# Performance work log

Measured on AMD Instinct MI355X. Metric: run time of the kernel, lower is better.

Reference implementation:

```python
import jax, jax.numpy as jnp
import numpy as np

N, E, F_IN, H, O = 50000, 800000, 128, 64, 1


def _gcn_conv(x, row, col, ew, W, b, n_nodes):
    """PyG GCNConv: add self-loops (weight 1), symmetric deg normalization,
    linear transform (no bias inside lin), scatter-add aggregation, then +bias."""
    loop = jnp.arange(n_nodes, dtype=row.dtype)
    r = jnp.concatenate([row, loop])
    c = jnp.concatenate([col, loop])
    w = jnp.concatenate([ew, jnp.ones((n_nodes,), dtype=ew.dtype)])
    deg = jax.ops.segment_sum(w, c, num_segments=n_nodes)            # [N]
    dis = jnp.where(deg > 0, jax.lax.rsqrt(jnp.maximum(deg, 1e-12)), 0.0)
    norm = dis[r] * w * dis[c]                                       # [E+N]
    h = x @ W                                                        # [N, out]
    msg = h[r] * norm[:, None]                                       # gather + scale
    agg = jax.ops.segment_sum(msg, c, num_segments=n_nodes)          # scatter-add
    return agg + b


def setup_inputs() -> dict:
    key = jax.random.key(0)
    ks = jax.random.split(key, 14)
    s = 0.02
    return {
        "x": jax.random.normal(ks[0], (N, F_IN), dtype=jnp.float32),
        "edge_index": jax.random.randint(ks[1], (2, E), 0, N, dtype=jnp.int64),
        "edge_weight": jax.random.uniform(ks[2], (E,), dtype=jnp.float32),
        "W1": jax.random.normal(ks[3], (F_IN, H), dtype=jnp.float32) * s,
        "b1": jnp.zeros((H,), dtype=jnp.float32),
        "W2": jax.random.normal(ks[4], (H, H), dtype=jnp.float32) * s,
        "b2": jnp.zeros((H,), dtype=jnp.float32),
        "W_ih": jax.random.normal(ks[5], (4 * H, H), dtype=jnp.float32) * s,
        "W_hh": jax.random.normal(ks[6], (4 * H, H), dtype=jnp.float32) * s,
        "b_ih": jax.random.normal(ks[7], (4 * H,), dtype=jnp.float32) * s,
        "b_hh": jax.random.normal(ks[8], (4 * H,), dtype=jnp.float32) * s,
        "W_reg": jax.random.normal(ks[9], (H, O), dtype=jnp.float32) * s,
        "b_reg": jnp.zeros((O,), dtype=jnp.float32),
    }


def reference(x, edge_index, edge_weight, W1, b1, W2, b2,
              W_ih, W_hh, b_ih, b_hh, W_reg, b_reg):
    row, col = edge_index[0], edge_index[1]
    n = x.shape[0]
    h = jax.nn.relu(_gcn_conv(x, row, col, edge_weight, W1, b1, n))
    h = jax.nn.relu(_gcn_conv(h, row, col, edge_weight, W2, b2, n))
    # single-step LSTM, zero initial (h0, c0); PyTorch gate order i, f, g, o
    hd = W_ih.shape[1]
    h0 = jnp.zeros((n, hd), dtype=h.dtype)
    gates = h @ W_ih.T + h0 @ W_hh.T + b_ih + b_hh                   # [N, 4H]
    i, f, g, o = jnp.split(gates, 4, axis=-1)
    c = jax.nn.sigmoid(f) * 0.0 + jax.nn.sigmoid(i) * jnp.tanh(g)    # c0 = 0
    hn = jax.nn.sigmoid(o) * jnp.tanh(c)                             # lstm_out[:, -1]
    return hn @ W_reg + b_reg
```

## Files before the change

kernel.cpp:

```cpp
#include <hip/hip_runtime.h>
#include <math.h>


#define QN 6272
#define NOCT 8
#define NPAD (NOCT * QN)
#define NSLICE 128
#define HIST_BLOCKS (NSLICE * NOCT)

__device__ __forceinline__ float sigmoidf_(float x) {
    return 1.0f / (1.0f + expf(-x));
}

__global__ __launch_bounds__(256) void hist_gemm1_k(
        const int* __restrict__ col, unsigned short* __restrict__ part,
        int E, int N,
        const float* __restrict__ x, const float* __restrict__ W1,
        float* __restrict__ C) {
    extern __shared__ char smem[];
    const int t = threadIdx.x;
    if (blockIdx.x < HIST_BLOCKS) {
        int* hc = (int*)smem;
        const int s = blockIdx.x >> 3;
        const int q = blockIdx.x & 7;
        const int lo = q * QN;
        for (int i = t; i < QN; i += 256) hc[i] = 0;
        __syncthreads();
        const int per = (E + NSLICE - 1) / NSLICE;
        const int e0 = s * per, e1 = min(E, e0 + per);
        int e = e0 + t;
        for (; e + 768 < e1; e += 1024) {
            int c0 = col[e], c1 = col[e + 256], c2 = col[e + 512], c3 = col[e + 768];
            unsigned r0 = (unsigned)(c0 - lo), r1 = (unsigned)(c1 - lo);
            unsigned r2 = (unsigned)(c2 - lo), r3 = (unsigned)(c3 - lo);
            if (r0 < (unsigned)QN && (unsigned)c0 < (unsigned)N) atomicAdd(&hc[r0], 1);
            if (r1 < (unsigned)QN && (unsigned)c1 < (unsigned)N) atomicAdd(&hc[r1], 1);
            if (r2 < (unsigned)QN && (unsigned)c2 < (unsigned)N) atomicAdd(&hc[r2], 1);
            if (r3 < (unsigned)QN && (unsigned)c3 < (unsigned)N) atomicAdd(&hc[r3], 1);
        }
        for (; e < e1; e += 256) {
            int c = col[e];
            unsigned rel = (unsigned)(c - lo);
            if (rel < (unsigned)QN && (unsigned)c < (unsigned)N) atomicAdd(&hc[rel], 1);
        }
        __syncthreads();
        unsigned short* dst = part + (size_t)s * NPAD + lo;
        for (int i = t; i < QN; i += 256) dst[i] = (unsigned short)hc[i];
    } else {
        float (*xs)[68] = (float (*)[68])smem;
        float* ws = (float*)(smem + 64 * 68 * sizeof(float));
        const int n0 = (int)(blockIdx.x - HIST_BLOCKS) * 64;
        for (int base = t * 4; base < 128 * 64; base += 1024)
            *(float4*)(ws + base) = *(const float4*)(W1 + base);
        const int cg = t & 15, ng = t >> 4;
        const int colj = cg * 4, nb = ng * 4;
        float acc[4][4];
#pragma unroll
        for (int i = 0; i < 4; ++i)
#pragma unroll
            for (int j = 0; j < 4; ++j) acc[i][j] = 0.0f;
        for (int k0 = 0; k0 < 128; k0 += 64) {
            __syncthreads();
            for (int base = t * 4; base < 64 * 64; base += 1024) {
                int r = base >> 6, k = base & 63;
                int node = n0 + r;
                float4 v = make_float4(0.f, 0.f, 0.f, 0.f);
                if (node < N) v = *(const float4*)(x + (size_t)node * 128 + k0 + k);
                *(float4*)&xs[r][k] = v;
            }
            __syncthreads();
#pragma unroll 4
            for (int kk = 0; kk < 64; kk += 4) {
                float4 a[4];
#pragma unroll
                for (int i = 0; i < 4; ++i) a[i] = *(float4*)&xs[nb + i][kk];
#pragma unroll
                for (int j = 0; j < 4; ++j) {
                    float4 bv = *(float4*)&ws[(size_t)(k0 + kk + j) * 64 + colj];
                    float av[4];
                    switch (j) {
                        case 0: av[0]=a[0].x; av[1]=a[1].x; av[2]=a[2].x; av[3]=a[3].x; break;
                        case 1: av[0]=a[0].y; av[1]=a[1].y; av[2]=a[2].y; av[3]=a[3].y; break;
                        case 2: av[0]=a[0].z; av[1]=a[1].z; av[2]=a[2].z; av[3]=a[3].z; break;
                        default:av[0]=a[0].w; av[1]=a[1].w; av[2]=a[2].w; av[3]=a[3].w; break;
                    }
#pragma unroll
                    for (int i = 0; i < 4; ++i) {
                        acc[i][0] = fmaf(av[i], bv.x, acc[i][0]);
                        acc[i][1] = fmaf(av[i], bv.y, acc[i][1]);
                        acc[i][2] = fmaf(av[i], bv.z, acc[i][2]);
                        acc[i][3] = fmaf(av[i], bv.w, acc[i][3]);
                    }
                }
            }
        }
#pragma unroll
        for (int i = 0; i < 4; ++i) {
            int node = n0 + nb + i;
            if (node < N)
                *(float4*)(C + (size_t)node * 64 + colj) =
                    make_float4(acc[i][0], acc[i][1], acc[i][2], acc[i][3]);
        }
    }
}

__global__ __launch_bounds__(256) void prefixA_k(const unsigned short* __restrict__ part,
                                                 unsigned short* __restrict__ coff,
                                                 int* __restrict__ cnt,
                                                 int* __restrict__ bsum) {
    __shared__ int r[256];
    const int t = threadIdx.x;
    const int i = blockIdx.x * 256 + t;
    int acc = 0;
    for (int s = 0; s < NSLICE; ++s) {
        size_t idx = (size_t)s * NPAD + i;
        coff[idx] = (unsigned short)acc;
        acc += part[idx];
    }
    cnt[i] = acc;
    r[t] = acc;
    __syncthreads();
#pragma unroll
    for (int off = 128; off > 0; off >>= 1) {
        if (t < off) r[t] += r[t + off];
        __syncthreads();
    }
    if (t == 0) bsum[blockIdx.x] = r[0];
}

__global__ __launch_bounds__(256) void scanBC_k(const int* __restrict__ cnt,
                                                const int* __restrict__ bsum,
                                                int* __restrict__ rowptr, int NBLK) {
    __shared__ int s[2][256];
    __shared__ int red[256];
    const int t = threadIdx.x, b = blockIdx.x;
    const int i = b * 256 + t;
    int v = cnt[i];
    int pin = 0;
    s[0][t] = v;
    __syncthreads();
#pragma unroll
    for (int off = 1; off < 256; off <<= 1) {
        int xo = s[pin][t];
        if (t >= off) xo += s[pin][t - off];
        s[pin ^ 1][t] = xo;
        pin ^= 1;
        __syncthreads();
    }
    int excl = s[pin][t] - v;
    red[t] = (t < b && t < NBLK) ? bsum[t] : 0;
    __syncthreads();
#pragma unroll
    for (int off = 128; off > 0; off >>= 1) {
        if (t < off) red[t] += red[t + off];
        __syncthreads();
    }
    rowptr[i] = excl + red[0];
}

__global__ __launch_bounds__(256) void fill_k(const int* __restrict__ row,
                                              const int* __restrict__ col,
                                              const float* __restrict__ ew,
                                              const int* __restrict__ rowptr,
                                              const unsigned short* __restrict__ coff,
                                              int2* __restrict__ pairs, int E, int N) {
    __shared__ int lcur[QN];
    const int t = threadIdx.x;
    const int s = blockIdx.x >> 3;
    const int q = blockIdx.x & 7;
    const int lo = q * QN;
    const unsigned short* cof = coff + (size_t)s * NPAD + lo;
    const int* rp = rowptr + lo;
    for (int i = t; i < QN; i += 256) lcur[i] = rp[i] + (int)cof[i];
    __syncthreads();
    const int per = (E + NSLICE - 1) / NSLICE;
    const int e0 = s * per, e1 = min(E, e0 + per);
    int e = e0 + t;
    for (; e + 768 < e1; e += 1024) {
        int c0 = col[e], c1 = col[e + 256], c2 = col[e + 512], c3 = col[e + 768];
        unsigned r0 = (unsigned)(c0 - lo), r1 = (unsigned)(c1 - lo);
        unsigned r2 = (unsigned)(c2 - lo), r3 = (unsigned)(c3 - lo);
        if (r0 < (unsigned)QN && (unsigned)c0 < (unsigned)N) {
            int r = row[e]; float w = ew[e];
            if ((unsigned)r >= (unsigned)N) { r = 0; w = 0.0f; }
            pairs[atomicAdd(&lcur[r0], 1)] = make_int2(r, __float_as_int(w));
        }
        if (r1 < (unsigned)QN && (unsigned)c1 < (unsigned)N) {
            int r = row[e + 256]; float w = ew[e + 256];
            if ((unsigned)r >= (unsigned)N) { r = 0; w = 0.0f; }
            pairs[atomicAdd(&lcur[r1], 1)] = make_int2(r, __float_as_int(w));
        }
        if (r2 < (unsigned)QN && (unsigned)c2 < (unsigned)N) {
            int r = row[e + 512]; float w = ew[e + 512];
            if ((unsigned)r >= (unsigned)N) { r = 0; w = 0.0f; }
            pairs[atomicAdd(&lcur[r2], 1)] = make_int2(r, __float_as_int(w));
        }
        if (r3 < (unsigned)QN && (unsigned)c3 < (unsigned)N) {
            int r = row[e + 768]; float w = ew[e + 768];
            if ((unsigned)r >= (unsigned)N) { r = 0; w = 0.0f; }
            pairs[atomicAdd(&lcur[r3], 1)] = make_int2(r, __float_as_int(w));
        }
    }
    for (; e < e1; e += 256) {
        int c = col[e];
        unsigned rel = (unsigned)(c - lo);
        if (rel < (unsigned)QN && (unsigned)c < (unsigned)N) {
            int r = row[e]; float w = ew[e];
            if ((unsigned)r >= (unsigned)N) { r = 0; w = 0.0f; }
            pairs[atomicAdd(&lcur[rel], 1)] = make_int2(r, __float_as_int(w));
        }
    }
}

__global__ __launch_bounds__(256) void degsum_k(const int* __restrict__ rowptr,
                                                const int2* __restrict__ pairs,
                                                float* __restrict__ dis, int N) {
    int i = blockIdx.x * 256 + threadIdx.x;
    if (i >= N) return;
    int b = rowptr[i], en = rowptr[i + 1];
    float s = 0.0f;
    for (int e = b; e < en; ++e) s += __int_as_float(pairs[e].y);
    dis[i] = rsqrtf(s + 1.0f);
}

__global__ __launch_bounds__(256) void aggregate_k(const float* __restrict__ h,
                                                   const int* __restrict__ rowptr,
                                                   const int2* __restrict__ pairs,
                                                   const float* __restrict__ dis,
                                                   const float* __restrict__ bias,
                                                   float* __restrict__ out, int N) {
    __shared__ int2 pl[4][4][64];
    const int t = threadIdx.x;
    const int lane = t & 63, w = t >> 6;
    const int n0 = (blockIdx.x * 4 + w) * 4;
    if (n0 >= N) return;

    int rp[5];
#pragma unroll
    for (int k = 0; k < 5; ++k) rp[k] = rowptr[min(n0 + k, N)];
    int len[4]; int L = 0;
#pragma unroll
    for (int i = 0; i < 4; ++i) { len[i] = rp[i + 1] - rp[i]; L = max(L, len[i]); }

    float acc[4] = {0.f, 0.f, 0.f, 0.f};
    for (int base = 0; base < L; base += 64) {
#pragma unroll
        for (int i = 0; i < 4; ++i) {
            int m = len[i] - base;
            int2 p = make_int2(0, 0);
            if (lane < m) {
                p = pairs[rp[i] + base + lane];
                p.y = __float_as_int(__int_as_float(p.y) * dis[p.x]);
            }
            pl[w][i][lane] = p;
        }
        const int m = min(64, L - base);
        int j = 0;
        for (; j + 4 <= m; j += 4) {
#pragma unroll
            for (int jj = 0; jj < 4; ++jj) {
                int2 p0 = pl[w][0][j + jj];
                int2 p1 = pl[w][1][j + jj];
                int2 p2 = pl[w][2][j + jj];
                int2 p3 = pl[w][3][j + jj];
                float h0 = h[(size_t)p0.x * 64 + lane];
                float h1 = h[(size_t)p1.x * 64 + lane];
                float h2 = h[(size_t)p2.x * 64 + lane];
                float h3 = h[(size_t)p3.x * 64 + lane];
                acc[0] = fmaf(h0, __int_as_float(p0.y), acc[0]);
                acc[1] = fmaf(h1, __int_as_float(p1.y), acc[1]);
                acc[2] = fmaf(h2, __int_as_float(p2.y), acc[2]);
                acc[3] = fmaf(h3, __int_as_float(p3.y), acc[3]);
            }
        }
        for (; j < m; ++j) {
            int2 p0 = pl[w][0][j];
            int2 p1 = pl[w][1][j];
            int2 p2 = pl[w][2][j];
            int2 p3 = pl[w][3][j];
            acc[0] = fmaf(h[(size_t)p0.x * 64 + lane], __int_as_float(p0.y), acc[0]);
            acc[1] = fmaf(h[(size_t)p1.x * 64 + lane], __int_as_float(p1.y), acc[1]);
            acc[2] = fmaf(h[(size_t)p2.x * 64 + lane], __int_as_float(p2.y), acc[2]);
            acc[3] = fmaf(h[(size_t)p3.x * 64 + lane], __int_as_float(p3.y), acc[3]);
        }
    }
#pragma unroll
    for (int i = 0; i < 4; ++i) {
        int node = n0 + i;
        if (node < N) {
            float d = dis[node];
            float a = acc[i];
            a = fmaf(d, h[(size_t)node * 64 + lane], a);
            a = fmaf(d, a, bias[lane]);
            out[(size_t)node * 64 + lane] = fmaxf(a, 0.0f);
        }
    }
}

template <int K>
__global__ __launch_bounds__(256) void gemm64_k(const float* __restrict__ A,
                                                const float* __restrict__ W,
                                                float* __restrict__ C, int M) {
    __shared__ float xs[64][68];
    __shared__ float ws[K][64];
    const int t  = threadIdx.x;
    const int n0 = blockIdx.x * 64;

    for (int base = t * 4; base < K * 64; base += 1024)
        *(float4*)((float*)ws + base) = *(const float4*)(W + base);

    const int cg = t & 15, ng = t >> 4;
    const int col = cg * 4, nb = ng * 4;
    float acc[4][4];
#pragma unroll
    for (int i = 0; i < 4; ++i)
#pragma unroll
        for (int j = 0; j < 4; ++j) acc[i][j] = 0.0f;

    for (int k0 = 0; k0 < K; k0 += 64) {
        __syncthreads();
        for (int base = t * 4; base < 64 * 64; base += 1024) {
            int r = base >> 6, k = base & 63;
            int node = n0 + r;
            float4 v = make_float4(0.f, 0.f, 0.f, 0.f);
            if (node < M) v = *(const float4*)(A + (size_t)node * K + k0 + k);
            *(float4*)&xs[r][k] = v;
        }
        __syncthreads();
#pragma unroll 4
        for (int kk = 0; kk < 64; kk += 4) {
            float4 a[4];
#pragma unroll
            for (int i = 0; i < 4; ++i) a[i] = *(float4*)&xs[nb + i][kk];
#pragma unroll
            for (int j = 0; j < 4; ++j) {
                float4 bv = *(float4*)&ws[k0 + kk + j][col];
                float av[4];
                switch (j) {
                    case 0: av[0]=a[0].x; av[1]=a[1].x; av[2]=a[2].x; av[3]=a[3].x; break;
                    case 1: av[0]=a[0].y; av[1]=a[1].y; av[2]=a[2].y; av[3]=a[3].y; break;
                    case 2: av[0]=a[0].z; av[1]=a[1].z; av[2]=a[2].z; av[3]=a[3].z; break;
                    default:av[0]=a[0].w; av[1]=a[1].w; av[2]=a[2].w; av[3]=a[3].w; break;
                }
#pragma unroll
                for (int i = 0; i < 4; ++i) {
                    acc[i][0] = fmaf(av[i], bv.x, acc[i][0]);
                    acc[i][1] = fmaf(av[i], bv.y, acc[i][1]);
                    acc[i][2] = fmaf(av[i], bv.z, acc[i][2]);
                    acc[i][3] = fmaf(av[i], bv.w, acc[i][3]);
                }
            }
        }
    }
#pragma unroll
    for (int i = 0; i < 4; ++i) {
        int node = n0 + nb + i;
        if (node < M)
            *(float4*)(C + (size_t)node * 64 + col) =
                make_float4(acc[i][0], acc[i][1], acc[i][2], acc[i][3]);
    }
}

__global__ __launch_bounds__(256) void lstm_head_k(const float* __restrict__ h,
                                                   const float* __restrict__ Wih,
                                                   const float* __restrict__ bih,
                                                   const float* __restrict__ bhh,
                                                   const float* __restrict__ Wreg,
                                                   const float* __restrict__ breg,
                                                   float* __restrict__ out, int N) {
    __shared__ float wt[64 * 192];
    __shared__ float hsT[64 * 64];
    const int t = threadIdx.x;
    const int n0 = blockIdx.x * 64;

    {
        const int j = t & 63, kq = (t >> 6) * 4;
#pragma unroll
        for (int gid = 0; gid < 3; ++gid) {
            const int gBase = (gid == 0) ? 0 : (gid == 1 ? 128 : 192);
            const int gOff = gid * 64;
#pragma unroll
            for (int it = 0; it < 4; ++it) {
                int k0 = it * 16 + kq;
                float4 w = *(const float4*)(Wih + (size_t)(gBase + j) * 64 + k0);
                wt[(k0 + 0) * 192 + gOff + j] = w.x;
                wt[(k0 + 1) * 192 + gOff + j] = w.y;
                wt[(k0 + 2) * 192 + gOff + j] = w.z;
                wt[(k0 + 3) * 192 + gOff + j] = w.w;
            }
        }
    }
    {
        const int r = t & 63, kq = (t >> 6) * 4;
        const int node = n0 + r;
#pragma unroll
        for (int it = 0; it < 4; ++it) {
            int k0 = it * 16 + kq;
            float4 v = make_float4(0.f, 0.f, 0.f, 0.f);
            if (node < N) v = *(const float4*)(h + (size_t)node * 64 + k0);
            hsT[(k0 + 0) * 64 + r] = v.x;
            hsT[(k0 + 1) * 64 + r] = v.y;
            hsT[(k0 + 2) * 64 + r] = v.z;
            hsT[(k0 + 3) * 64 + r] = v.w;
        }
    }

    const int cg = t & 15, ng = t >> 4;
    const int col = cg * 4, nb = ng * 4;
    float4 bi4 = *(const float4*)(bih + col);
    float4 bg4 = *(const float4*)(bih + 128 + col);
    float4 bo4 = *(const float4*)(bih + 192 + col);
    {
        float4 h0 = *(const float4*)(bhh + col);
        float4 h1 = *(const float4*)(bhh + 128 + col);
        float4 h2 = *(const float4*)(bhh + 192 + col);
        bi4.x += h0.x; bi4.y += h0.y; bi4.z += h0.z; bi4.w += h0.w;
        bg4.x += h1.x; bg4.y += h1.y; bg4.z += h1.z; bg4.w += h1.w;
        bo4.x += h2.x; bo4.y += h2.y; bo4.z += h2.z; bo4.w += h2.w;
    }
    float4 wr4 = *(const float4*)(Wreg + col);
    const float br = breg[0];

    __syncthreads();

    float ai[4][4], ag[4][4], ao[4][4];
#pragma unroll
    for (int i = 0; i < 4; ++i)
#pragma unroll
        for (int j = 0; j < 4; ++j) { ai[i][j] = 0.f; ag[i][j] = 0.f; ao[i][j] = 0.f; }

#pragma unroll 4
    for (int k = 0; k < 64; ++k) {
        float4 a  = *(float4*)&hsT[k * 64 + nb];
        float4 wi = *(float4*)&wt[k * 192 + col];
        float4 wg = *(float4*)&wt[k * 192 + 64 + col];
        float4 wo = *(float4*)&wt[k * 192 + 128 + col];
        const float av[4] = {a.x, a.y, a.z, a.w};
#pragma unroll
        for (int i = 0; i < 4; ++i) {
            ai[i][0] = fmaf(av[i], wi.x, ai[i][0]);
            ai[i][1] = fmaf(av[i], wi.y, ai[i][1]);
            ai[i][2] = fmaf(av[i], wi.z, ai[i][2]);
            ai[i][3] = fmaf(av[i], wi.w, ai[i][3]);
            ag[i][0] = fmaf(av[i], wg.x, ag[i][0]);
            ag[i][1] = fmaf(av[i], wg.y, ag[i][1]);
            ag[i][2] = fmaf(av[i], wg.z, ag[i][2]);
            ag[i][3] = fmaf(av[i], wg.w, ag[i][3]);
            ao[i][0] = fmaf(av[i], wo.x, ao[i][0]);
            ao[i][1] = fmaf(av[i], wo.y, ao[i][1]);
            ao[i][2] = fmaf(av[i], wo.z, ao[i][2]);
            ao[i][3] = fmaf(av[i], wo.w, ao[i][3]);
        }
    }

    const float bia[4] = {bi4.x, bi4.y, bi4.z, bi4.w};
    const float bga[4] = {bg4.x, bg4.y, bg4.z, bg4.w};
    const float boa[4] = {bo4.x, bo4.y, bo4.z, bo4.w};
    const float wra[4] = {wr4.x, wr4.y, wr4.z, wr4.w};
    float res[4];
#pragma unroll
    for (int i = 0; i < 4; ++i) {
        float s = 0.f;
#pragma unroll
        for (int j = 0; j < 4; ++j) {
            float gi = ai[i][j] + bia[j];
            float gg = ag[i][j] + bga[j];
            float go = ao[i][j] + boa[j];
            float cc = sigmoidf_(gi) * tanhf(gg);
            float hn = sigmoidf_(go) * tanhf(cc);
            s = fmaf(hn, wra[j], s);
        }
        res[i] = s;
    }
#pragma unroll
    for (int off = 8; off > 0; off >>= 1) {
#pragma unroll
        for (int i = 0; i < 4; ++i) res[i] += __shfl_down(res[i], off);
    }
    if (cg == 0) {
#pragma unroll
        for (int i = 0; i < 4; ++i) {
            int node = n0 + nb + i;
            if (node < N) out[node] = res[i] + br;
        }
    }
}

extern "C" void kernel_launch(void* const* d_in, const int* in_sizes, int n_in,
                              void* d_out, int out_size, void* d_ws, size_t ws_size,
                              hipStream_t stream) {
    const float* x    = (const float*)d_in[0];
    const int*   ei   = (const int*)d_in[1];
    const float* ew   = (const float*)d_in[2];
    const float* W1   = (const float*)d_in[3];
    const float* b1   = (const float*)d_in[4];
    const float* W2   = (const float*)d_in[5];
    const float* b2   = (const float*)d_in[6];
    const float* Wih  = (const float*)d_in[7];
    const float* bih  = (const float*)d_in[9];
    const float* bhh  = (const float*)d_in[10];
    const float* Wreg = (const float*)d_in[11];
    const float* breg = (const float*)d_in[12];
    float* out = (float*)d_out;

    const int N = out_size;
    const int E = in_sizes[1] / 2;
    const int* row = ei;
    const int* col = ei + E;

    const int NB   = (N + 255) / 256;
    const int NBLK = NPAD / 256;

    char* wsb = (char*)d_ws;
    size_t off = 0;
    unsigned short* part = (unsigned short*)(wsb + off); off += (size_t)NSLICE * NPAD * 2;
    unsigned short* coff = (unsigned short*)(wsb + off); off += (size_t)NSLICE * NPAD * 2;
    float* bufA   = (float*)(wsb + off); off += (size_t)N * 64 * 4;
    float* bufB   = (float*)(wsb + off); off += (size_t)N * 64 * 4;
    float* bufC   = (float*)(wsb + off); off += (size_t)N * 64 * 4;
    int2*  pairs  = (int2*) (wsb + off); off += (size_t)E * 8;
    float* dis    = (float*)(wsb + off); off += (size_t)NPAD * 4;
    int*   cnt    = (int*)  (wsb + off); off += (size_t)NPAD * 4;
    int*   rowptr = (int*)  (wsb + off); off += ((size_t)NPAD + 64) * 4;
    int*   bsum   = (int*)  (wsb + off); off += 1024;

    const int gb = (N + 63) / 64;
    const int ab = (N + 15) / 16;
    const size_t DSM = 64 * 68 * sizeof(float) + 128 * 64 * sizeof(float);

    hist_gemm1_k<<<HIST_BLOCKS + gb, 256, DSM, stream>>>(col, part, E, N, x, W1, bufA);
    prefixA_k<<<NBLK, 256, 0, stream>>>(part, coff, cnt, bsum);
    scanBC_k<<<NBLK, 256, 0, stream>>>(cnt, bsum, rowptr, NBLK);
    fill_k<<<HIST_BLOCKS, 256, 0, stream>>>(row, col, ew, rowptr, coff, pairs, E, N);
    degsum_k<<<NB, 256, 0, stream>>>(rowptr, pairs, dis, N);
    aggregate_k<<<ab, 256, 0, stream>>>(bufA, rowptr, pairs, dis, b1, bufB, N);
    gemm64_k<64><<<gb, 256, 0, stream>>>(bufB, W2, bufC, N);
    aggregate_k<<<ab, 256, 0, stream>>>(bufC, rowptr, pairs, dis, b2, bufA, N);
    lstm_head_k<<<gb, 256, 0, stream>>>(bufA, Wih, bih, bhh, Wreg, breg, out, N);
}
```

Measured before the change: 280.9 us.

## Aggregate over a contiguous 4-node edge range with readlane broadcasts instead of LDS

The aggregation kernel now treats the four nodes' CSR edges as one contiguous range and loads 64 edges per chunk with no padding to the longest node. Edge indices and scaled weights are broadcast to the wave with readlane instead of being staged through shared memory. This removes LDS traffic and the wasted work on shorter nodes. The cost is a serial per-node inner loop with a single accumulator chain, which reduces independent gathers in flight compared to the old four-node interleave.

```diff
diff --git a/kernel.cpp b/kernel.cpp
--- a/kernel.cpp
+++ b/kernel.cpp
@@ -229,59 +229,54 @@
                                                    const float* __restrict__ dis,
                                                    const float* __restrict__ bias,
                                                    float* __restrict__ out, int N) {
-    __shared__ int2 pl[4][4][64];
     const int t = threadIdx.x;
-    const int lane = t & 63, w = t >> 6;
-    const int n0 = (blockIdx.x * 4 + w) * 4;
+    const int lane = t & 63;
+    const int n0 = (blockIdx.x * 4 + (t >> 6)) * 4;
     if (n0 >= N) return;
 
     int rp[5];
 #pragma unroll
     for (int k = 0; k < 5; ++k) rp[k] = rowptr[min(n0 + k, N)];
-    int len[4]; int L = 0;
-#pragma unroll
-    for (int i = 0; i < 4; ++i) { len[i] = rp[i + 1] - rp[i]; L = max(L, len[i]); }
+    const int beg = rp[0], end = rp[4];
 
     float acc[4] = {0.f, 0.f, 0.f, 0.f};
-    for (int base = 0; base < L; base += 64) {
+    for (int base = beg; base < end; base += 64) {
+        const int m = min(64, end - base);
+        int ps = 0; float pv = 0.0f;
+        if (lane < m) {
+            int2 p = pairs[base + lane];
+            ps = p.x;
+            pv = __int_as_float(p.y) * dis[p.x];
+        }
+        const unsigned pu = __float_as_uint(pv);
 #pragma unroll
         for (int i = 0; i < 4; ++i) {
-            int m = len[i] - base;
-            int2 p = make_int2(0, 0);
-            if (lane < m) {
-                p = pairs[rp[i] + base + lane];
-                p.y = __float_as_int(__int_as_float(p.y) * dis[p.x]);
+            const int s0 = max(rp[i] - base, 0);
+            const int s1 = min(rp[i + 1] - base, m);
+            int jj = s0;
+            for (; jj + 4 <= s1; jj += 4) {
+                int a0 = __builtin_amdgcn_readlane(ps, jj);
+                int a1 = __builtin_amdgcn_readlane(ps, jj + 1);
+                int a2 = __builtin_amdgcn_readlane(ps, jj + 2);
+                int a3 = __builtin_amdgcn_readlane(ps, jj + 3);
+                float v0 = __uint_as_float(__builtin_amdgcn_readlane(pu, jj));
+                float v1 = __uint_as_float(__builtin_amdgcn_readlane(pu, jj + 1));
+                float v2 = __uint_as_float(__builtin_amdgcn_readlane(pu, jj + 2));
+                float v3 = __uint_as_float(__builtin_amdgcn_readlane(pu, jj + 3));
+                float h0 = h[(size_t)a0 * 64 + lane];
+                float h1 = h[(size_t)a1 * 64 + lane];
+                float h2 = h[(size_t)a2 * 64 + lane];
+                float h3 = h[(size_t)a3 * 64 + lane];
+                acc[i] = fmaf(h0, v0, acc[i]);
+                acc[i] = fmaf(h1, v1, acc[i]);
+                acc[i] = fmaf(h2, v2, acc[i]);
+                acc[i] = fmaf(h3, v3, acc[i]);
             }
-            pl[w][i][lane] = p;
-        }
-        const int m = min(64, L - base);
-        int j = 0;
-        for (; j + 4 <= m; j += 4) {
-#pragma unroll
-            for (int jj = 0; jj < 4; ++jj) {
-                int2 p0 = pl[w][0][j + jj];
-                int2 p1 = pl[w][1][j + jj];
-                int2 p2 = pl[w][2][j + jj];
-                int2 p3 = pl[w][3][j + jj];
-                float h0 = h[(size_t)p0.x * 64 + lane];
-                float h1 = h[(size_t)p1.x * 64 + lane];
-                float h2 = h[(size_t)p2.x * 64 + lane];
-                float h3 = h[(size_t)p3.x * 64 + lane];
-                acc[0] = fmaf(h0, __int_as_float(p0.y), acc[0]);
-                acc[1] = fmaf(h1, __int_as_float(p1.y), acc[1]);
-                acc[2] = fmaf(h2, __int_as_float(p2.y), acc[2]);
-                acc[3] = fmaf(h3, __int_as_float(p3.y), acc[3]);
+            for (; jj < s1; ++jj) {
+                int   a0 = __builtin_amdgcn_readlane(ps, jj);
+                float v0 = __uint_as_float(__builtin_amdgcn_readlane(pu, jj));
+                acc[i] = fmaf(h[(size_t)a0 * 64 + lane], v0, acc[i]);
             }
-        }
-        for (; j < m; ++j) {
-            int2 p0 = pl[w][0][j];
-            int2 p1 = pl[w][1][j];
-            int2 p2 = pl[w][2][j];
-            int2 p3 = pl[w][3][j];
-            acc[0] = fmaf(h[(size_t)p0.x * 64 + lane], __int_as_float(p0.y), acc[0]);
-            acc[1] = fmaf(h[(size_t)p1.x * 64 + lane], __int_as_float(p1.y), acc[1]);
-            acc[2] = fmaf(h[(size_t)p2.x * 64 + lane], __int_as_float(p2.y), acc[2]);
-            acc[3] = fmaf(h[(size_t)p3.x * 64 + lane], __int_as_float(p3.y), acc[3]);
         }
     }
 #pragma unroll
```

New measurement: 272.2 us. -3.1%, faster.
